# Kernel optimization log

Measured on AMD Instinct MI355X. Metric: run time of the kernel, lower is better.

Reference implementation:

```python
import jax, jax.numpy as jnp
import numpy as np

N = 100000   # nodes
E = 200000   # edges
L = 3        # GNN layers
D = 300      # node feature dim
H = 150      # per-direction message dim


def setup_inputs() -> dict:
    key = jax.random.key(0)
    ks = jax.random.split(key, 8)
    s = 0.05
    return {
        "x": jax.random.normal(ks[0], (N, D), jnp.float32),
        "edge_index": jax.random.randint(ks[1], (2, E), 0, N, dtype=jnp.int32),
        "Wr": jax.random.normal(ks[2], (L, 2 * D, H), jnp.float32) * s,
        "br": jax.random.normal(ks[3], (L, H), jnp.float32) * s,
        "Wc": jax.random.normal(ks[4], (L, 2 * D, H), jnp.float32) * s,
        "bc": jax.random.normal(ks[5], (L, H), jnp.float32) * s,
        "Wa": jax.random.normal(ks[6], (D, D), jnp.float32) * s,
        "ba": jax.random.normal(ks[7], (D,), jnp.float32) * s,
    }


def _gelu(z):
    return jax.nn.gelu(z, approximate=False)  # torch GELU is exact erf


def _msg_aggr(v, src, dst, W, b):
    # message at each edge: GELU(Linear(cat(x_i, x_j))), x_i = target, x_j = source
    m = _gelu(jnp.concatenate([v[dst], v[src]], axis=-1) @ W + b)  # [E, H]
    # sum-aggregate messages at target nodes
    return jax.ops.segment_sum(m, dst, num_segments=N)  # [N, H]


def reference(x, edge_index, Wr, br, Wc, bc, Wa, ba):
    src, dst = edge_index[0], edge_index[1]

    def step(v, p):
        Wr_l, br_l, Wc_l, bc_l = p
        r = _msg_aggr(v, src, dst, Wr_l, br_l)        # r2c: original direction
        c = _msg_aggr(v, dst, src, Wc_l, bc_l)        # c2r: flipped edge_index
        v = v + _gelu(jnp.concatenate([r, c], axis=-1) @ Wa + ba)
        return v, None

    out, _ = jax.lax.scan(step, x, (Wr, br, Wc, bc))
    return out
```

## Files before the change

kernel.cpp:

```cpp
#include <hip/hip_runtime.h>
#include <hip/hip_bf16.h>
#include <math.h>

#define NND 100000
#define EE  200000
#define LL  3
#define DD  300
#define HH  150

#define MPAD 100096
#define KP   320
#define NPJ  640
#define NUP  384
#define NTK  (KP / 32)

#define NB   49
#define SCN  (NB * 2048)

#define BSTRIDE 132

typedef __attribute__((ext_vector_type(8))) short bf16x8;
typedef __attribute__((ext_vector_type(4))) short bf16x4;
typedef __attribute__((ext_vector_type(4))) float f32x4;

__device__ __forceinline__ float gelu_exact(float z) {
    return 0.5f * z * (1.0f + erff(z * 0.7071067811865475f));
}
__device__ __forceinline__ unsigned short f2bf(float f) {
    union { float fv; unsigned u; } v; v.fv = f;
    unsigned r = v.u + 0x7fff + ((v.u >> 16) & 1);
    return (unsigned short)(r >> 16);
}
__device__ __forceinline__ float bf2f(unsigned short b) {
    union { unsigned u; float fv; } v; v.u = ((unsigned)b) << 16;
    return v.fv;
}

__global__ __launch_bounds__(256) void pack_w(
    const float* __restrict__ Wr, const float* __restrict__ Wc,
    const float* __restrict__ Wa,
    unsigned short* __restrict__ Bt, unsigned short* __restrict__ Wat)
{
    int i = blockIdx.x * 256 + threadIdx.x;
    const int btTotal = LL * NPJ * KP;
    if (i < btTotal) {
        int l = i / (NPJ * KP);
        int rem = i % (NPJ * KP);
        int n = rem / KP;
        int k = rem % KP;
        float v = 0.f;
        if (k < DD && n < 600) {
            const float* W = (n < 300) ? Wr : Wc;
            int nn = (n < 300) ? n : n - 300;
            int krow = (nn < 150) ? k : 300 + k;
            int j    = (nn < 150) ? nn : nn - 150;
            v = W[(size_t)l * 600 * 150 + (size_t)krow * 150 + j];
        }
        Bt[i] = f2bf(v);
    } else {
        int i2 = i - btTotal;
        if (i2 < NUP * KP) {
            int n = i2 / KP, k = i2 % KP;
            float v = (n < DD && k < DD) ? Wa[(size_t)k * DD + n] : 0.f;
            Wat[i2] = f2bf(v);
        }
    }
}

__global__ __launch_bounds__(256) void init_vbf(
    const float* __restrict__ x, unsigned short* __restrict__ vbf)
{
    int idx = blockIdx.x * 256 + threadIdx.x;
    int row = idx / (KP / 8);
    int gk  = (idx % (KP / 8)) * 8;
    if (row >= MPAD) return;
    unsigned short tmp[8];
    if (row < NND && gk < DD) {
        if (gk + 8 <= DD) {
            const float4* p = (const float4*)(x + (size_t)row * DD + gk);
            float4 f0 = p[0], f1 = p[1];
            tmp[0] = f2bf(f0.x); tmp[1] = f2bf(f0.y);
            tmp[2] = f2bf(f0.z); tmp[3] = f2bf(f0.w);
            tmp[4] = f2bf(f1.x); tmp[5] = f2bf(f1.y);
            tmp[6] = f2bf(f1.z); tmp[7] = f2bf(f1.w);
        } else {
            #pragma unroll
            for (int j = 0; j < 8; ++j)
                tmp[j] = (gk + j < DD) ? f2bf(x[(size_t)row * DD + gk + j]) : 0;
        }
    } else {
        #pragma unroll
        for (int j = 0; j < 8; ++j) tmp[j] = 0;
    }
    *((bf16x8*)&vbf[(size_t)row * KP + gk]) = *((bf16x8*)tmp);
}

__global__ __launch_bounds__(256) void hist_deg(
    const int* __restrict__ src, const int* __restrict__ dst,
    int* __restrict__ deg)
{
    int e = blockIdx.x * 256 + threadIdx.x;
    if (e >= EE) return;
    atomicAdd(&deg[dst[e]], 1);
    atomicAdd(&deg[SCN + src[e]], 1);
}

__global__ __launch_bounds__(256) void scanA(
    const int* __restrict__ deg, int* __restrict__ off, int* __restrict__ bsum)
{
    __shared__ int ls[256];
    const int t = threadIdx.x, row = blockIdx.y;
    const int base = blockIdx.x * 2048 + t * 8;
    const int* dg = deg + (size_t)row * SCN + base;
    int v[8];
    #pragma unroll
    for (int j = 0; j < 8; ++j) v[j] = dg[j];
    int tot = 0;
    #pragma unroll
    for (int j = 0; j < 8; ++j) tot += v[j];
    ls[t] = tot;
    __syncthreads();
    #pragma unroll
    for (int d = 1; d < 256; d <<= 1) {
        int tv = (t >= d) ? ls[t - d] : 0;
        __syncthreads();
        ls[t] += tv;
        __syncthreads();
    }
    int run = ls[t] - tot;
    int* op = off + (size_t)row * SCN + base;
    #pragma unroll
    for (int j = 0; j < 8; ++j) { op[j] = run; run += v[j]; }
    if (t == 255) bsum[row * 64 + blockIdx.x] = ls[255];
}

__global__ __launch_bounds__(256) void scanB(int* __restrict__ bsum)
{
    if (threadIdx.x < 2) {
        int row = threadIdx.x, c = 0;
        for (int i = 0; i < NB; ++i) {
            int tv = bsum[row * 64 + i];
            bsum[row * 64 + i] = c;
            c += tv;
        }
    }
}

__global__ __launch_bounds__(256) void scanC(
    int* __restrict__ off, const int* __restrict__ bsum, int* __restrict__ cur)
{
    const int t = threadIdx.x, row = blockIdx.y;
    const int base = blockIdx.x * 2048 + t * 8;
    const int add = bsum[row * 64 + blockIdx.x];
    int* op = off + (size_t)row * SCN + base;
    int* cp = cur + (size_t)row * SCN + base;
    #pragma unroll
    for (int j = 0; j < 8; ++j) {
        int v = op[j] + add;
        op[j] = v;
        cp[j] = v;
    }
}

__global__ __launch_bounds__(256) void fill_adj(
    const int* __restrict__ src, const int* __restrict__ dst,
    int* __restrict__ cur, int* __restrict__ adj)
{
    int e = blockIdx.x * 256 + threadIdx.x;
    if (e >= EE) return;
    int s = src[e], d = dst[e];
    int pd = atomicAdd(&cur[d], 1);
    adj[pd] = s;
    int ps = atomicAdd(&cur[SCN + s], 1);
    adj[EE + ps] = d;
}

__global__ __launch_bounds__(256) void aggregate(
    const int* __restrict__ off, const int* __restrict__ adj,
    const unsigned short* __restrict__ P,
    const float* __restrict__ br, const float* __restrict__ bc,
    unsigned short* __restrict__ RC)
{
    const int n    = blockIdx.x * 4 + (threadIdx.x >> 6);
    const int dir  = blockIdx.y;
    const int lane = threadIdx.x & 63;
    const int h0 = lane, h1 = lane + 64, h2 = lane + 128;

    unsigned short* outrow = RC + (size_t)n * KP + dir * 150;
    if (n >= NND) {
        outrow[h0] = 0; outrow[h1] = 0;
        if (h2 < (dir ? 170 : 150)) outrow[h2] = 0;
        return;
    }

    const int* offp = off + (size_t)dir * SCN;
    const int* adjp = adj + (size_t)dir * EE;
    const float* bias = dir ? bc : br;
    const unsigned short* own = P + (size_t)n * NPJ + dir * 300;
    const int poff = dir ? 450 : 150;

    float o0 = bf2f(own[h0]) + bias[h0];
    float o1 = bf2f(own[h1]) + bias[h1];
    float o2 = (h2 < 150) ? bf2f(own[h2]) + bias[h2] : 0.f;

    float s0 = 0.f, s1 = 0.f, s2 = 0.f;
    int beg = offp[n], end = offp[n + 1];
    for (int i = beg; i < end; ++i) {
        const unsigned short* pp = P + (size_t)adjp[i] * NPJ + poff;
        s0 += gelu_exact(o0 + bf2f(pp[h0]));
        s1 += gelu_exact(o1 + bf2f(pp[h1]));
        if (h2 < 150) s2 += gelu_exact(o2 + bf2f(pp[h2]));
    }
    outrow[h0] = f2bf(s0);
    outrow[h1] = f2bf(s1);
    if (h2 < 150)                  outrow[h2] = f2bf(s2);
    else if (dir == 1 && h2 < 170) outrow[h2] = 0;
}

#define GLOAD16(gp, lp) __builtin_amdgcn_global_load_lds( \
    (const __attribute__((address_space(1))) unsigned int*)(gp), \
    (__attribute__((address_space(3))) unsigned int*)(lp), 16, 0, 0)

#define STAGE_LDS(dstp, srcbase, rowoff, k0) do {                            \
    _Pragma("unroll")                                                        \
    for (int i_ = 0; i_ < 2; ++i_) {                                         \
        int cb_ = wid * 128 + i_ * 64;                                       \
        int ci_ = cb_ + lane;                                                \
        int row_ = ci_ >> 2, pc_ = ci_ & 3;                                  \
        int c_ = pc_ ^ ((row_ >> 1) & 3);                                    \
        GLOAD16(srcbase + (size_t)(rowoff + row_) * KP + (k0) + c_ * 8,      \
                &(dstp)[cb_ * 8]);                                           \
    } } while (0)

template<int MODE>
__global__ __launch_bounds__(256) void gemm_mfma(
    const unsigned short* __restrict__ Ab,
    const unsigned short* __restrict__ Bt,
    unsigned short* __restrict__ P,
    float* __restrict__ outv, unsigned short* __restrict__ vbf,
    const float* __restrict__ bias, int last)
{
    __shared__ char smem[4 * 16384];
    float* bounce = (float*)smem;

    const int tid  = threadIdx.x;
    const int lane = tid & 63;
    const int wid  = tid >> 6;

    const int gx   = gridDim.x;
    const int nwg  = gx * gridDim.y;
    const int flat = blockIdx.y * gx + blockIdx.x;
    const int q = nwg >> 3, r = nwg & 7;
    const int xcd = flat & 7, off = flat >> 3;
    const int lid = (xcd < r ? xcd * (q + 1) : r * (q + 1) + (xcd - r) * q) + off;
    const int brow = (lid / gx) * 128;
    const int bcol = (lid % gx) * 128;

    const int wm = (wid >> 1) * 64;
    const int wn = (wid & 1) * 64;

    f32x4 acc[4][4];
    #pragma unroll
    for (int i = 0; i < 4; ++i)
        #pragma unroll
        for (int j = 0; j < 4; ++j)
            #pragma unroll
            for (int rr = 0; rr < 4; ++rr) acc[i][j][rr] = 0.f;

    #pragma unroll
    for (int t = 0; t < 2; ++t) {
        unsigned short* Al = (unsigned short*)(smem + t * 16384);
        unsigned short* Bl = (unsigned short*)(smem + t * 16384 + 8192);
        STAGE_LDS(Al, Ab, brow, t * 32);
        STAGE_LDS(Bl, Bt, bcol, t * 32);
    }

    #pragma unroll
    for (int t = 0; t < NTK; ++t) {
        const int b = t & 3;
        unsigned short* Alc = (unsigned short*)(smem + b * 16384);
        unsigned short* Blc = (unsigned short*)(smem + b * 16384 + 8192);
        if (t + 2 < NTK) {
            const int bn = (t + 2) & 3;
            unsigned short* Aln = (unsigned short*)(smem + bn * 16384);
            unsigned short* Bln = (unsigned short*)(smem + bn * 16384 + 8192);
            STAGE_LDS(Aln, Ab, brow, (t + 2) * 32);
            STAGE_LDS(Bln, Bt, bcol, (t + 2) * 32);
            asm volatile("s_waitcnt vmcnt(8)" ::: "memory");
        } else if (t + 1 < NTK) {
            asm volatile("s_waitcnt vmcnt(4)" ::: "memory");
        } else {
            asm volatile("s_waitcnt vmcnt(0)" ::: "memory");
        }
        __builtin_amdgcn_s_barrier();

        bf16x8 af[4], bfr[4];
        #pragma unroll
        for (int mi = 0; mi < 4; ++mi) {
            int row = wm + mi * 16 + (lane & 15);
            af[mi] = *((const bf16x8*)&Alc[row * 32 + (((lane >> 4) ^ ((row >> 1) & 3)) * 8)]);
        }
        #pragma unroll
        for (int nj = 0; nj < 4; ++nj) {
            int row = wn + nj * 16 + (lane & 15);
            bfr[nj] = *((const bf16x8*)&Blc[row * 32 + (((lane >> 4) ^ ((row >> 1) & 3)) * 8)]);
        }
        __builtin_amdgcn_s_setprio(1);
        #pragma unroll
        for (int mi = 0; mi < 4; ++mi)
            #pragma unroll
            for (int nj = 0; nj < 4; ++nj)
                acc[mi][nj] = __builtin_amdgcn_mfma_f32_16x16x32_bf16(
                    af[mi], bfr[nj], acc[mi][nj], 0, 0, 0);
        __builtin_amdgcn_s_setprio(0);
    }
    __builtin_amdgcn_s_barrier();

    const int ro = tid >> 5;
    const int co = (tid & 31) * 4;
    #pragma unroll
    for (int half = 0; half < 2; ++half) {
        if (wm == half * 64) {
            #pragma unroll
            for (int mi = 0; mi < 4; ++mi)
                #pragma unroll
                for (int nj = 0; nj < 4; ++nj) {
                    int lcol = wn + nj * 16 + (lane & 15);
                    int rb = mi * 16 + ((lane >> 4) << 2);
                    #pragma unroll
                    for (int rr = 0; rr < 4; ++rr)
                        bounce[(rb + rr) * BSTRIDE + lcol] = acc[mi][nj][rr];
                }
        }
        __syncthreads();
        #pragma unroll
        for (int i = 0; i < 8; ++i) {
            int lrow = ro + i * 8;
            int grow = brow + half * 64 + lrow;
            float4 vv = *(const float4*)&bounce[lrow * BSTRIDE + co];
            if (MODE == 0) {
                bf16x4 o;
                o[0] = (short)f2bf(vv.x); o[1] = (short)f2bf(vv.y);
                o[2] = (short)f2bf(vv.z); o[3] = (short)f2bf(vv.w);
                *((bf16x4*)&P[(size_t)grow * NPJ + bcol + co]) = o;
            } else if (grow < NND) {
                int gc = bcol + co;
                if (bcol < 256) {
                    float4 bv = *(const float4*)&bias[gc];
                    bf16x4 old = *(const bf16x4*)&vbf[(size_t)grow * KP + gc];
                    float4 nv;
                    nv.x = bf2f((unsigned short)old[0]) + gelu_exact(vv.x + bv.x);
                    nv.y = bf2f((unsigned short)old[1]) + gelu_exact(vv.y + bv.y);
                    nv.z = bf2f((unsigned short)old[2]) + gelu_exact(vv.z + bv.z);
                    nv.w = bf2f((unsigned short)old[3]) + gelu_exact(vv.w + bv.w);
                    if (last) {
                        *((float4*)&outv[(size_t)grow * DD + gc]) = nv;
                    } else {
                        bf16x4 o;
                        o[0] = (short)f2bf(nv.x); o[1] = (short)f2bf(nv.y);
                        o[2] = (short)f2bf(nv.z); o[3] = (short)f2bf(nv.w);
                        *((bf16x4*)&vbf[(size_t)grow * KP + gc]) = o;
                    }
                } else {
                    #pragma unroll
                    for (int j = 0; j < 4; ++j) {
                        int c = gc + j;
                        if (c < DD) {
                            float vj = (j == 0) ? vv.x : (j == 1) ? vv.y
                                     : (j == 2) ? vv.z : vv.w;
                            size_t vidx = (size_t)grow * KP + c;
                            float nv = bf2f(vbf[vidx]) + gelu_exact(vj + bias[c]);
                            if (last) outv[(size_t)grow * DD + c] = nv;
                            else      vbf[vidx] = f2bf(nv);
                        }
                    }
                }
            }
        }
        __syncthreads();
    }
}

extern "C" void kernel_launch(void* const* d_in, const int* in_sizes, int n_in,
                              void* d_out, int out_size, void* d_ws, size_t ws_size,
                              hipStream_t stream) {
    const float* x  = (const float*)d_in[0];
    const int*   ei = (const int*)  d_in[1];
    const float* Wr = (const float*)d_in[2];
    const float* br = (const float*)d_in[3];
    const float* Wc = (const float*)d_in[4];
    const float* bc = (const float*)d_in[5];
    const float* Wa = (const float*)d_in[6];
    const float* ba = (const float*)d_in[7];
    float* out = (float*)d_out;

    const size_t P_elems   = (size_t)MPAD * NPJ;
    const size_t RC_elems  = (size_t)MPAD * KP;
    const size_t V_elems   = (size_t)MPAD * KP;
    const size_t Bt_elems  = (size_t)LL * NPJ * KP;
    const size_t Wat_elems = (size_t)NUP * KP;

    unsigned short* P   = (unsigned short*)d_ws;
    unsigned short* RC  = P + P_elems;
    unsigned short* vbf = RC + RC_elems;
    unsigned short* Bt  = vbf + V_elems;
    unsigned short* Wat = Bt + Bt_elems;
    int* deg  = (int*)(Wat + Wat_elems);
    int* off  = deg + 2 * SCN;
    int* curp = off + 2 * SCN;
    int* adj  = curp + 2 * SCN;
    int* bsum = adj + 2 * EE;
    const size_t need = (char*)(bsum + 128) - (char*)d_ws;
    if (ws_size < need) return;

    pack_w<<<2880, 256, 0, stream>>>(Wr, Wc, Wa, Bt, Wat);
    init_vbf<<<(int)((V_elems / 8 + 255) / 256), 256, 0, stream>>>(x, vbf);

    const int* src = ei;
    const int* dst = ei + EE;

    hipMemsetAsync(deg, 0, 2 * SCN * sizeof(int), stream);
    hist_deg<<<(EE + 255) / 256, 256, 0, stream>>>(src, dst, deg);
    scanA<<<dim3(NB, 2), 256, 0, stream>>>(deg, off, bsum);
    scanB<<<1, 256, 0, stream>>>(bsum);
    scanC<<<dim3(NB, 2), 256, 0, stream>>>(off, bsum, curp);
    fill_adj<<<(EE + 255) / 256, 256, 0, stream>>>(src, dst, curp, adj);

    dim3 gproj(NPJ / 128, MPAD / 128);
    dim3 gupd (NUP / 128, MPAD / 128);
    dim3 gagg (MPAD / 4, 2);

    for (int l = 0; l < LL; ++l) {
        gemm_mfma<0><<<gproj, 256, 0, stream>>>(
            vbf, Bt + (size_t)l * NPJ * KP, P, nullptr, nullptr, nullptr, 0);
        aggregate<<<gagg, 256, 0, stream>>>(
            off, adj, P, br + (size_t)l * HH, bc + (size_t)l * HH, RC);
        gemm_mfma<1><<<gupd, 256, 0, stream>>>(
            RC, Wat, nullptr, out, vbf, ba, (l == LL - 1) ? 1 : 0);
    }
}
```

Baseline: 1.029 ms.

## Realign projection layout for vectorized aggregation and deepen GEMM prefetch

Reorders the packed projection columns so each direction's per-source and per-target halves start at 8-byte-aligned offsets, and pads the RC buffer so the second direction starts at column 160. Wa is repacked to match that padding. The aggregate kernel then uses one 4-wide bf16 load per lane per edge instead of three scalar loads, and prefetches the next adjacency index. The GEMM pipeline now prefetches three k-tiles ahead and issues the loads after the barrier, trading more outstanding memory ops for better latency hiding.

```diff
diff --git a/kernel.cpp b/kernel.cpp
--- a/kernel.cpp
+++ b/kernel.cpp
@@ -18,6 +18,13 @@
 #define SCN  (NB * 2048)
 
 #define BSTRIDE 132
+
+#define P_BR 0
+#define P_BC 152
+#define P_AR 304
+#define P_AC 456
+#define RC_R 0
+#define RC_C 160
 
 typedef __attribute__((ext_vector_type(8))) short bf16x8;
 typedef __attribute__((ext_vector_type(4))) short bf16x4;
@@ -49,19 +56,24 @@
         int n = rem / KP;
         int k = rem % KP;
         float v = 0.f;
-        if (k < DD && n < 600) {
-            const float* W = (n < 300) ? Wr : Wc;
-            int nn = (n < 300) ? n : n - 300;
-            int krow = (nn < 150) ? k : 300 + k;
-            int j    = (nn < 150) ? nn : nn - 150;
-            v = W[(size_t)l * 600 * 150 + (size_t)krow * 150 + j];
+        if (k < DD) {
+            const float* W = nullptr; int krow = k, j = -1;
+            if (n >= P_BR && n < P_BR + 150)      { W = Wr; krow = 300 + k; j = n - P_BR; }
+            else if (n >= P_BC && n < P_BC + 150) { W = Wc; krow = 300 + k; j = n - P_BC; }
+            else if (n >= P_AR && n < P_AR + 150) { W = Wr; krow = k;       j = n - P_AR; }
+            else if (n >= P_AC && n < P_AC + 150) { W = Wc; krow = k;       j = n - P_AC; }
+            if (j >= 0)
+                v = W[(size_t)l * 600 * 150 + (size_t)krow * 150 + j];
         }
         Bt[i] = f2bf(v);
     } else {
         int i2 = i - btTotal;
         if (i2 < NUP * KP) {
             int n = i2 / KP, k = i2 % KP;
-            float v = (n < DD && k < DD) ? Wa[(size_t)k * DD + n] : 0.f;
+            int kk = -1;
+            if (k < 150)                 kk = k;
+            else if (k >= 160 && k < 310) kk = k - 10;
+            float v = (n < DD && kk >= 0) ? Wa[(size_t)kk * DD + n] : 0.f;
             Wat[i2] = f2bf(v);
         }
     }
@@ -184,37 +196,52 @@
     const int n    = blockIdx.x * 4 + (threadIdx.x >> 6);
     const int dir  = blockIdx.y;
     const int lane = threadIdx.x & 63;
-    const int h0 = lane, h1 = lane + 64, h2 = lane + 128;
-
-    unsigned short* outrow = RC + (size_t)n * KP + dir * 150;
-    if (n >= NND) {
-        outrow[h0] = 0; outrow[h1] = 0;
-        if (h2 < (dir ? 170 : 150)) outrow[h2] = 0;
-        return;
-    }
+    const int c    = lane * 4;
+
+    if (lane < 10)
+        RC[(size_t)n * KP + (dir ? 310 : 150) + lane] = 0;
+    if (c >= 152) return;
 
     const int* offp = off + (size_t)dir * SCN;
     const int* adjp = adj + (size_t)dir * EE;
     const float* bias = dir ? bc : br;
-    const unsigned short* own = P + (size_t)n * NPJ + dir * 300;
-    const int poff = dir ? 450 : 150;
-
-    float o0 = bf2f(own[h0]) + bias[h0];
-    float o1 = bf2f(own[h1]) + bias[h1];
-    float o2 = (h2 < 150) ? bf2f(own[h2]) + bias[h2] : 0.f;
-
-    float s0 = 0.f, s1 = 0.f, s2 = 0.f;
+    const unsigned short* own = P + (size_t)n * NPJ + (dir ? P_AC : P_AR);
+    const int poff = dir ? P_BC : P_BR;
+
+    const bool g0 = (c + 0) < 150, g1 = (c + 1) < 150;
+    const bool g2 = (c + 2) < 150, g3 = (c + 3) < 150;
+
+    bf16x4 ow = *((const bf16x4*)&own[c]);
+    float o0 = bf2f((unsigned short)ow[0]) + (g0 ? bias[c + 0] : 0.f);
+    float o1 = bf2f((unsigned short)ow[1]) + (g1 ? bias[c + 1] : 0.f);
+    float o2 = bf2f((unsigned short)ow[2]) + (g2 ? bias[c + 2] : 0.f);
+    float o3 = bf2f((unsigned short)ow[3]) + (g3 ? bias[c + 3] : 0.f);
+
+    float s0 = 0.f, s1 = 0.f, s2 = 0.f, s3 = 0.f;
     int beg = offp[n], end = offp[n + 1];
-    for (int i = beg; i < end; ++i) {
-        const unsigned short* pp = P + (size_t)adjp[i] * NPJ + poff;
-        s0 += gelu_exact(o0 + bf2f(pp[h0]));
-        s1 += gelu_exact(o1 + bf2f(pp[h1]));
-        if (h2 < 150) s2 += gelu_exact(o2 + bf2f(pp[h2]));
-    }
-    outrow[h0] = f2bf(s0);
-    outrow[h1] = f2bf(s1);
-    if (h2 < 150)                  outrow[h2] = f2bf(s2);
-    else if (dir == 1 && h2 < 170) outrow[h2] = 0;
+    if (beg < end) {
+        int a = adjp[beg];
+        for (int i = beg; i < end; ++i) {
+            int anext = (i + 1 < end) ? adjp[i + 1] : 0;
+            const unsigned short* pp = P + (size_t)a * NPJ + poff;
+            bf16x4 pv = *((const bf16x4*)&pp[c]);
+            s0 += gelu_exact(o0 + bf2f((unsigned short)pv[0]));
+            s1 += gelu_exact(o1 + bf2f((unsigned short)pv[1]));
+            s2 += gelu_exact(o2 + bf2f((unsigned short)pv[2]));
+            s3 += gelu_exact(o3 + bf2f((unsigned short)pv[3]));
+            a = anext;
+        }
+    }
+    unsigned short* outrow = RC + (size_t)n * KP + (dir ? RC_C : RC_R);
+    if (c + 4 <= 150) {
+        bf16x4 o;
+        o[0] = (short)f2bf(s0); o[1] = (short)f2bf(s1);
+        o[2] = (short)f2bf(s2); o[3] = (short)f2bf(s3);
+        *((bf16x4*)&outrow[c]) = o;
+    } else {
+        if (g0) outrow[c + 0] = f2bf(s0);
+        if (g1) outrow[c + 1] = f2bf(s1);
+    }
 }
 
 #define GLOAD16(gp, lp) __builtin_amdgcn_global_load_lds( \
@@ -268,7 +295,7 @@
             for (int rr = 0; rr < 4; ++rr) acc[i][j][rr] = 0.f;
 
     #pragma unroll
-    for (int t = 0; t < 2; ++t) {
+    for (int t = 0; t < 3; ++t) {
         unsigned short* Al = (unsigned short*)(smem + t * 16384);
         unsigned short* Bl = (unsigned short*)(smem + t * 16384 + 8192);
         STAGE_LDS(Al, Ab, brow, t * 32);
@@ -280,19 +307,21 @@
         const int b = t & 3;
         unsigned short* Alc = (unsigned short*)(smem + b * 16384);
         unsigned short* Blc = (unsigned short*)(smem + b * 16384 + 8192);
-        if (t + 2 < NTK) {
-            const int bn = (t + 2) & 3;
-            unsigned short* Aln = (unsigned short*)(smem + bn * 16384);
-            unsigned short* Bln = (unsigned short*)(smem + bn * 16384 + 8192);
-            STAGE_LDS(Aln, Ab, brow, (t + 2) * 32);
-            STAGE_LDS(Bln, Bt, bcol, (t + 2) * 32);
+        if (t <= NTK - 3) {
             asm volatile("s_waitcnt vmcnt(8)" ::: "memory");
-        } else if (t + 1 < NTK) {
+        } else if (t == NTK - 2) {
             asm volatile("s_waitcnt vmcnt(4)" ::: "memory");
         } else {
             asm volatile("s_waitcnt vmcnt(0)" ::: "memory");
         }
         __builtin_amdgcn_s_barrier();
+        if (t + 3 < NTK) {
+            const int bn = (t + 3) & 3;
+            unsigned short* Aln = (unsigned short*)(smem + bn * 16384);
+            unsigned short* Bln = (unsigned short*)(smem + bn * 16384 + 8192);
+            STAGE_LDS(Aln, Ab, brow, (t + 3) * 32);
+            STAGE_LDS(Bln, Bt, bcol, (t + 3) * 32);
+        }
 
         bf16x8 af[4], bfr[4];
         #pragma unroll
@@ -364,13 +393,13 @@
                 } else {
                     #pragma unroll
                     for (int j = 0; j < 4; ++j) {
-                        int c = gc + j;
-                        if (c < DD) {
+                        int ccc = gc + j;
+                        if (ccc < DD) {
                             float vj = (j == 0) ? vv.x : (j == 1) ? vv.y
                                      : (j == 2) ? vv.z : vv.w;
-                            size_t vidx = (size_t)grow * KP + c;
-                            float nv = bf2f(vbf[vidx]) + gelu_exact(vj + bias[c]);
-                            if (last) outv[(size_t)grow * DD + c] = nv;
+                            size_t vidx = (size_t)grow * KP + ccc;
+                            float nv = bf2f(vbf[vidx]) + gelu_exact(vj + bias[ccc]);
+                            if (last) outv[(size_t)grow * DD + ccc] = nv;
                             else      vbf[vidx] = f2bf(nv);
                         }
                     }
```

Result: faster. 954.9 us (-7.2%).
